# Optimization experiments

Measured on AMD Instinct MI355X. Metric: run time of the kernel, lower is better.

## Reference

```python
import jax, jax.numpy as jnp
import numpy as np
from jax import lax

SEQ, HIS, TGT = 4096, 32768, 2048
LOC_E, TIM_E, HID, UID_E, UID_N = 512, 64, 512, 64, 100000
IN = LOC_E + TIM_E  # 576


def setup_inputs() -> dict:
    key = jax.random.key(0)
    ks = jax.random.split(key, 16)
    s = lambda *sh: 1.0 / np.sqrt(sh[-1])
    return {
        "loc_emb": jax.random.normal(ks[0], (SEQ, 1, LOC_E), jnp.float32),
        "tim_emb": jax.random.normal(ks[1], (SEQ, 1, TIM_E), jnp.float32),
        "history_loc_emb": jax.random.normal(ks[2], (HIS, 1, LOC_E), jnp.float32),
        "history_tim_emb": jax.random.normal(ks[3], (HIS, 1, TIM_E), jnp.float32),
        "history_count": jax.random.randint(ks[4], (HIS,), 0, 10),
        "uid": jax.random.randint(ks[5], (TGT,), 0, UID_N),
        "target_len": TGT,
        "batch_size": 1,
        "fc_attn_w": jax.random.normal(ks[6], (HID, IN), jnp.float32) * s(HID, IN),
        "fc_attn_b": jnp.zeros((HID,), jnp.float32),
        "w_ih": jax.random.normal(ks[7], (3 * HID, IN), jnp.float32) * s(3 * HID, IN),
        "w_hh": jax.random.normal(ks[8], (3 * HID, HID), jnp.float32) * s(3 * HID, HID),
        "b_ih": jnp.zeros((3 * HID,), jnp.float32),
        "b_hh": jnp.zeros((3 * HID,), jnp.float32),
        "emb_uid": jax.random.normal(ks[9], (UID_N, UID_E), jnp.float32),
        "fc_final_w": jax.random.normal(ks[10], (LOC_E, 2 * HID + UID_E), jnp.float32) * s(LOC_E, 2 * HID + UID_E),
        "fc_final_b": jnp.zeros((LOC_E,), jnp.float32),
    }


def reference(loc_emb, tim_emb, history_loc_emb, history_tim_emb, history_count,
              uid, target_len, batch_size, fc_attn_w, fc_attn_b,
              w_ih, w_hh, b_ih, b_hh, emb_uid, fc_final_w, fc_final_b):
    hid = w_hh.shape[1]
    # current trajectory input: (S, IN); batch dim is 1 -> squeeze
    x = jnp.concatenate([loc_emb, tim_emb], axis=2)[:, 0, :]
    # long-term history projected to hidden: (L, HID)
    hist = jnp.concatenate([history_loc_emb, history_tim_emb], axis=2)[:, 0, :]
    history = jnp.tanh(hist @ fc_attn_w.T + fc_attn_b)

    # GRU (PyTorch gate layout: r, z, n). Precompute input projections once.
    gi = x @ w_ih.T + b_ih  # (S, 3*HID)

    def step(h, gi_t):
        gh = h @ w_hh.T + b_hh
        i_r, i_z, i_n = jnp.split(gi_t, 3)
        h_r, h_z, h_n = jnp.split(gh, 3)
        r = jax.nn.sigmoid(i_r + h_r)
        z = jax.nn.sigmoid(i_z + h_z)
        n = jnp.tanh(i_n + r * h_n)
        h_new = (1.0 - z) * n + z * h
        return h_new, h_new

    h0 = jnp.zeros((hid,), x.dtype)
    _, out_state = lax.scan(step, h0, gi)  # (S, HID)

    q = out_state[-target_len:]                 # (T, HID)
    # dot-product attention over history (batched matmul instead of scalar loop)
    attn_w = jax.nn.softmax(q @ history.T, axis=1)   # (T, L)
    context = attn_w @ history                       # (T, HID)

    out = jnp.concatenate([q, context], axis=1)      # (T, 2*HID)
    uid_e = emb_uid[uid]                             # (T, UID_E)
    out = jnp.concatenate([out, uid_e], axis=1)
    y = out @ fc_final_w.T + fc_final_b              # (T, LOC_E)
    return jax.nn.log_softmax(y, axis=1)
```

## Files before the change

kernel.cpp:

```cpp
#include <hip/hip_runtime.h>

using short8  = __attribute__((ext_vector_type(8))) short;
using float4v = __attribute__((ext_vector_type(4))) float;

__device__ __forceinline__ unsigned short f2b(float f){
  unsigned u = __float_as_uint(f);
  u += 0x7FFFu + ((u >> 16) & 1u);
  return (unsigned short)(u >> 16);
}
__device__ __forceinline__ float b2f(unsigned short h){
  return __uint_as_float(((unsigned)h) << 16);
}
__device__ __forceinline__ float sigm(float x){ return 1.f/(1.f + __expf(-x)); }
__device__ __forceinline__ float tanh_f(float x){
  float cx = fminf(fmaxf(x, -15.f), 15.f);
  float e = __expf(2.f*cx);
  return (e - 1.f)/(e + 1.f);
}

#define SENT64 0x7F8000007F800000ULL

__global__ void ring_init(unsigned long long* ring){
  size_t i = (size_t)blockIdx.x*256 + threadIdx.x;
  if (i < 512) ring[i] = 0ull;
  else ring[i] = SENT64;
}

__global__ void cat_hist(const float* __restrict__ a, const float* __restrict__ b,
                         unsigned short* __restrict__ d){
  int r = blockIdx.x;
  const float* ar = a + (size_t)r*512;
  const float* br = b + (size_t)r*64;
  unsigned short* dr = d + (size_t)r*576;
  for (int c = threadIdx.x; c < 576; c += 64){
    float v = (c < 512) ? ar[c] : br[c-512];
    dr[c] = f2b(v);
  }
}

__global__ void cat_x3(const float* __restrict__ a, const float* __restrict__ b,
                       unsigned short* __restrict__ d){
  int r = blockIdx.x;
  const float* ar = a + (size_t)r*512;
  const float* br = b + (size_t)r*64;
  unsigned short* dr = d + (size_t)r*1728;
  for (int c = threadIdx.x; c < 576; c += 64){
    float v = (c < 512) ? ar[c] : br[c-512];
    unsigned short hi = f2b(v);
    unsigned short lo = f2b(v - b2f(hi));
    dr[c] = hi; dr[576+c] = lo; dr[1152+c] = hi;
  }
}

__global__ void cat_w3(const float* __restrict__ w, unsigned short* __restrict__ d){
  int r = blockIdx.x;
  const float* wr_ = w + (size_t)r*576;
  unsigned short* dr = d + (size_t)r*1728;
  for (int c = threadIdx.x; c < 576; c += 64){
    float v = wr_[c];
    unsigned short hi = f2b(v);
    unsigned short lo = f2b(v - b2f(hi));
    dr[c] = hi; dr[576+c] = hi; dr[1152+c] = lo;
  }
}

__global__ void cast_bf16_k(const float* __restrict__ s, unsigned short* __restrict__ d, int n){
  int i = blockIdx.x*256 + threadIdx.x;
  if (i < n) d[i] = f2b(s[i]);
}

__global__ void transpose_k(const unsigned short* __restrict__ src,
                            unsigned short* __restrict__ dst, int R, int C){
  __shared__ unsigned short t[32][33];
  int x = threadIdx.x & 31, y = threadIdx.x >> 5;
  int r0 = blockIdx.y*32, c0 = blockIdx.x*32;
  for (int p=0;p<4;++p) t[y+p*8][x] = src[(size_t)(r0+y+p*8)*C + c0+x];
  __syncthreads();
  for (int p=0;p<4;++p) dst[(size_t)(c0+y+p*8)*R + r0+x] = t[x][y+p*8];
}

__global__ void uid_gather(const int* __restrict__ uid, const float* __restrict__ emb,
                           unsigned short* __restrict__ outcat){
  int r = blockIdx.x, e = threadIdx.x;
  outcat[(size_t)r*1088 + 1024 + e] = f2b(emb[(size_t)uid[r]*64 + e]);
}

template<int ACT>
__global__ __launch_bounds__(256) void gemm_bt(
  const unsigned short* __restrict__ A, const unsigned short* __restrict__ B,
  const float* __restrict__ bias, float* __restrict__ Cf, unsigned short* __restrict__ Cb,
  int M, int N, int K)
{
  __shared__ unsigned short As[64*40];
  __shared__ unsigned short Bs[64*40];
  const int tid  = threadIdx.x;
  const int lane = tid & 63, wave = tid >> 6;
  const int wr = (wave>>1)*32, wc = (wave&1)*32;
  const int qa = lane>>4, la = lane&15;
  const int arow = tid>>2, acol = (tid&3)*8;
  const int tiles = K >> 5;
  const size_t abase = (size_t)(blockIdx.x*64 + arow)*K + acol;
  const size_t bbase = (size_t)(blockIdx.y*64 + arow)*K + acol;
  float4v acc[2][2] = {};
  short8 av = *(const short8*)(A + abase);
  short8 bv = *(const short8*)(B + bbase);
  for (int kt=0; kt<tiles; ++kt){
    __syncthreads();
    *(short8*)(As + arow*40 + acol) = av;
    *(short8*)(Bs + arow*40 + acol) = bv;
    __syncthreads();
    if (kt+1 < tiles){
      av = *(const short8*)(A + abase + (size_t)(kt+1)*32);
      bv = *(const short8*)(B + bbase + (size_t)(kt+1)*32);
    }
    short8 af0 = *(const short8*)(As + (wr+la)*40 + qa*8);
    short8 af1 = *(const short8*)(As + (wr+16+la)*40 + qa*8);
    short8 bf0 = *(const short8*)(Bs + (wc+la)*40 + qa*8);
    short8 bf1 = *(const short8*)(Bs + (wc+16+la)*40 + qa*8);
    acc[0][0] = __builtin_amdgcn_mfma_f32_16x16x32_bf16(af0, bf0, acc[0][0],0,0,0);
    acc[0][1] = __builtin_amdgcn_mfma_f32_16x16x32_bf16(af0, bf1, acc[0][1],0,0,0);
    acc[1][0] = __builtin_amdgcn_mfma_f32_16x16x32_bf16(af1, bf0, acc[1][0],0,0,0);
    acc[1][1] = __builtin_amdgcn_mfma_f32_16x16x32_bf16(af1, bf1, acc[1][1],0,0,0);
  }
  for (int mi=0;mi<2;++mi) for (int ni=0;ni<2;++ni){
    int n = blockIdx.y*64 + wc + ni*16 + la;
    float bvv = bias ? bias[n] : 0.f;
    for (int r=0;r<4;++r){
      int m = blockIdx.x*64 + wr + mi*16 + qa*4 + r;
      float v = acc[mi][ni][r] + bvv;
      if (ACT) v = tanh_f(v);
      if (Cf) Cf[(size_t)m*N + n] = v;
      if (Cb) Cb[(size_t)m*N + n] = f2b(v);
    }
  }
}

__global__ __launch_bounds__(64,1) void gru_scan(
  const float* __restrict__ gi, const float* __restrict__ whh, const float* __restrict__ bhh,
  unsigned long long* ring, unsigned short* __restrict__ outcat)
{
  const int lane = threadIdx.x;
  const int b = blockIdx.x;
  const int ob = b*8;
  float wgt[24][8];
  #pragma unroll
  for (int s=0; s<24; ++s){
    const float* wr_ = whh + (size_t)((s>>3)*512 + ob + (s&7))*512 + lane*8;
    #pragma unroll
    for (int m=0; m<8; ++m) wgt[s][m] = wr_[m];
  }
  float bh = 0.f;
  if (lane < 24) bh = bhh[(lane>>3)*512 + ob + (lane&7)];
  float hprev = 0.f;

  const int bit0=lane&1, bit1=(lane>>1)&1, bit2=(lane>>2)&1,
            bit3=(lane>>3)&1, bit4=(lane>>4)&1;

  for (int t=0; t<4096; ++t){
    float gval = 0.f;
    if (lane < 24) gval = gi[(size_t)t*1536 + (lane>>3)*512 + ob + (lane&7)];
    const unsigned long long* rc = ring + (size_t)t*512 + lane*8;
    unsigned long long a0,a1,a2,a3;
    for(;;){
      a0 = __hip_atomic_load(rc+0, __ATOMIC_RELAXED, __HIP_MEMORY_SCOPE_AGENT);
      a1 = __hip_atomic_load(rc+1, __ATOMIC_RELAXED, __HIP_MEMORY_SCOPE_AGENT);
      a2 = __hip_atomic_load(rc+2, __ATOMIC_RELAXED, __HIP_MEMORY_SCOPE_AGENT);
      a3 = __hip_atomic_load(rc+3, __ATOMIC_RELAXED, __HIP_MEMORY_SCOPE_AGENT);
      bool bad = (a0==SENT64)|(a1==SENT64)|(a2==SENT64)|(a3==SENT64);
      if (!__any(bad)) break;
    }
    float hv[8];
    hv[0]=__uint_as_float((unsigned)a0); hv[1]=__uint_as_float((unsigned)(a0>>32));
    hv[2]=__uint_as_float((unsigned)a1); hv[3]=__uint_as_float((unsigned)(a1>>32));
    hv[4]=__uint_as_float((unsigned)a2); hv[5]=__uint_as_float((unsigned)(a2>>32));
    hv[6]=__uint_as_float((unsigned)a3); hv[7]=__uint_as_float((unsigned)(a3>>32));
    float v[32];
    #pragma unroll
    for (int s=0; s<24; ++s){
      float acc = 0.f;
      #pragma unroll
      for (int m=0; m<8; ++m) acc += wgt[s][m]*hv[m];
      v[s] = acc;
    }
    #pragma unroll
    for (int s=24; s<32; ++s) v[s] = 0.f;
    float s16[16];
    #pragma unroll
    for (int j=0; j<16; ++j){
      float keep = bit0 ? v[2*j+1] : v[2*j];
      float send = bit0 ? v[2*j]   : v[2*j+1];
      s16[j] = keep + __shfl_xor(send, 1, 64);
    }
    float s8[8];
    #pragma unroll
    for (int j=0; j<8; ++j){
      float keep = bit1 ? s16[2*j+1] : s16[2*j];
      float send = bit1 ? s16[2*j]   : s16[2*j+1];
      s8[j] = keep + __shfl_xor(send, 2, 64);
    }
    float s4[4];
    #pragma unroll
    for (int j=0; j<4; ++j){
      float keep = bit2 ? s8[2*j+1] : s8[2*j];
      float send = bit2 ? s8[2*j]   : s8[2*j+1];
      s4[j] = keep + __shfl_xor(send, 4, 64);
    }
    float s2[2];
    #pragma unroll
    for (int j=0; j<2; ++j){
      float keep = bit3 ? s4[2*j+1] : s4[2*j];
      float send = bit3 ? s4[2*j]   : s4[2*j+1];
      s2[j] = keep + __shfl_xor(send, 8, 64);
    }
    {
      float keep = bit4 ? s2[1] : s2[0];
      float send = bit4 ? s2[0] : s2[1];
      s2[0] = keep + __shfl_xor(send, 16, 64);
    }
    float vsum = s2[0] + __shfl_xor(s2[0], 32, 64);
    float wsum = vsum + bh;
    float wrz  = wsum + gval;
    float uz  = __shfl(wrz,  lane+8,  64);
    float hn  = __shfl(wsum, lane+16, 64);
    float in_ = __shfl(gval, lane+16, 64);
    float hval = 0.f;
    if (lane < 8){
      float r = sigm(wrz);
      float z = sigm(uz);
      float n = tanh_f(in_ + r*hn);
      hval = (1.f - z)*n + z*hprev;
      hprev = hval;
    }
    float nb = __shfl_xor(hval, 1, 64);
    if (lane < 8 && !(lane & 1)){
      unsigned long long pack = (unsigned long long)__float_as_uint(hval)
                              | ((unsigned long long)__float_as_uint(nb) << 32);
      __hip_atomic_store(ring + (size_t)(t+1)*512 + b*8 + (lane>>1), pack,
                         __ATOMIC_RELAXED, __HIP_MEMORY_SCOPE_AGENT);
      if (t >= 2048){
        unsigned opack = (unsigned)f2b(hval) | ((unsigned)f2b(nb) << 16);
        *(unsigned*)(outcat + (size_t)(t-2048)*1088 + ob + lane) = opack;
      }
    }
  }
}

__global__ __launch_bounds__(256) void attn_stats(
  const unsigned short* __restrict__ Q, const unsigned short* __restrict__ H,
  float* __restrict__ mpart, float* __restrict__ lpart)
{
  __shared__ unsigned short qs[64*520];
  const int tid = threadIdx.x;
  const int lane = tid&63, wave = tid>>6;
  const int qa = lane>>4, la = lane&15;
  const int qt = blockIdx.x, sp = blockIdx.y;
  for (int p=0;p<16;++p){
    int idx = p*256 + tid;
    int row = idx>>6, c8 = (idx&63)*8;
    *(short8*)(qs + row*520 + c8) = *(const short8*)(Q + (size_t)(qt*64+row)*1088 + c8);
  }
  __syncthreads();
  const int rowbase = wave*16;
  float mrun[4] = {-3e38f,-3e38f,-3e38f,-3e38f};
  float lrun[4] = {0.f,0.f,0.f,0.f};
  for (int c=0;c<32;++c){
    int hb = sp*2048 + c*64;
    float4v sacc[4] = {};
    for (int ks=0; ks<16; ++ks){
      short8 af = *(const short8*)(qs + (rowbase+la)*520 + ks*32 + qa*8);
      #pragma unroll
      for (int ni=0; ni<4; ++ni){
        short8 bf = *(const short8*)(H + (size_t)(hb + ni*16 + la)*512 + ks*32 + qa*8);
        sacc[ni] = __builtin_amdgcn_mfma_f32_16x16x32_bf16(af, bf, sacc[ni],0,0,0);
      }
    }
    #pragma unroll
    for (int r=0;r<4;++r){
      float cm = fmaxf(fmaxf(sacc[0][r],sacc[1][r]), fmaxf(sacc[2][r],sacc[3][r]));
      cm = fmaxf(cm, __shfl_xor(cm,1,64));
      cm = fmaxf(cm, __shfl_xor(cm,2,64));
      cm = fmaxf(cm, __shfl_xor(cm,4,64));
      cm = fmaxf(cm, __shfl_xor(cm,8,64));
      float mnew = fmaxf(mrun[r], cm);
      float ls = __expf(sacc[0][r]-mnew)+__expf(sacc[1][r]-mnew)
               + __expf(sacc[2][r]-mnew)+__expf(sacc[3][r]-mnew);
      ls += __shfl_xor(ls,1,64); ls += __shfl_xor(ls,2,64);
      ls += __shfl_xor(ls,4,64); ls += __shfl_xor(ls,8,64);
      lrun[r] = lrun[r]*__expf(mrun[r]-mnew) + ls;
      mrun[r] = mnew;
    }
  }
  if (la == 0){
    #pragma unroll
    for (int r=0;r<4;++r){
      int row = qt*64 + rowbase + qa*4 + r;
      mpart[sp*2048 + row] = mrun[r];
      lpart[sp*2048 + row] = lrun[r];
    }
  }
}

__global__ void stats_combine(const float* __restrict__ mpart, const float* __restrict__ lpart,
                              float* __restrict__ mrow, float* __restrict__ lrow){
  int r = blockIdx.x*64 + threadIdx.x;
  float m = -3e38f;
  for (int s=0;s<16;++s) m = fmaxf(m, mpart[s*2048 + r]);
  float l = 0.f;
  for (int s=0;s<16;++s) l += lpart[s*2048 + r]*__expf(mpart[s*2048 + r] - m);
  mrow[r] = m; lrow[r] = l;
}

__global__ __launch_bounds__(256) void attn_ctx(
  const unsigned short* __restrict__ Q, const unsigned short* __restrict__ H,
  const unsigned short* __restrict__ Ht, const float* __restrict__ mrow,
  float* __restrict__ ctxpart)
{
  __shared__ unsigned short qs[64*520];
  __shared__ unsigned short ps[4*16*80];
  const int tid = threadIdx.x;
  const int lane = tid&63, wave = tid>>6;
  const int qa = lane>>4, la = lane&15;
  const int qt = blockIdx.x, sp = blockIdx.y;
  for (int p=0;p<16;++p){
    int idx = p*256 + tid;
    int row = idx>>6, c8 = (idx&63)*8;
    *(short8*)(qs + row*520 + c8) = *(const short8*)(Q + (size_t)(qt*64+row)*1088 + c8);
  }
  __syncthreads();
  const int rowbase = wave*16;
  float mreg[4];
  #pragma unroll
  for (int r=0;r<4;++r) mreg[r] = mrow[qt*64 + rowbase + qa*4 + r];
  float4v cacc[32] = {};
  unsigned short* pw = ps + wave*16*80;
  for (int c=0;c<64;++c){
    int hb = sp*4096 + c*64;
    float4v sacc[4] = {};
    for (int ks=0; ks<16; ++ks){
      short8 af = *(const short8*)(qs + (rowbase+la)*520 + ks*32 + qa*8);
      #pragma unroll
      for (int ni=0; ni<4; ++ni){
        short8 bf = *(const short8*)(H + (size_t)(hb + ni*16 + la)*512 + ks*32 + qa*8);
        sacc[ni] = __builtin_amdgcn_mfma_f32_16x16x32_bf16(af, bf, sacc[ni],0,0,0);
      }
    }
    #pragma unroll
    for (int ni=0;ni<4;++ni)
      #pragma unroll
      for (int r=0;r<4;++r)
        pw[(qa*4+r)*80 + ni*16 + la] = f2b(__expf(sacc[ni][r]-mreg[r]));
    #pragma unroll
    for (int ks2=0; ks2<2; ++ks2){
      short8 paf = *(const short8*)(pw + la*80 + ks2*32 + qa*8);
      for (int f=0; f<32; ++f){
        short8 bf = *(const short8*)(Ht + (size_t)(f*16+la)*32768 + hb + ks2*32 + qa*8);
        cacc[f] = __builtin_amdgcn_mfma_f32_16x16x32_bf16(paf, bf, cacc[f],0,0,0);
      }
    }
  }
  for (int f=0; f<32; ++f)
    #pragma unroll
    for (int r=0;r<4;++r){
      int row = qt*64 + rowbase + qa*4 + r;
      ctxpart[((size_t)sp*2048 + row)*512 + f*16 + la] = cacc[f][r];
    }
}

__global__ void ctx_reduce(const float* __restrict__ ctxpart, const float* __restrict__ lrow,
                           unsigned short* __restrict__ outcat){
  int idx = blockIdx.x*256 + threadIdx.x;
  int r = idx >> 9, cc = idx & 511;
  float s = 0.f;
  for (int sp=0; sp<8; ++sp) s += ctxpart[((size_t)sp*2048 + r)*512 + cc];
  outcat[(size_t)r*1088 + 512 + cc] = f2b(s / lrow[r]);
}

__global__ void log_softmax_k(const float* __restrict__ y, float* __restrict__ out){
  int r = blockIdx.x, lane = threadIdx.x;
  const float* yr = y + (size_t)r*512;
  float v[8]; float m = -3e38f;
  #pragma unroll
  for (int i=0;i<8;++i){ v[i] = yr[lane + 64*i]; m = fmaxf(m, v[i]); }
  #pragma unroll
  for (int d=1; d<64; d<<=1) m = fmaxf(m, __shfl_xor(m,d,64));
  float s = 0.f;
  #pragma unroll
  for (int i=0;i<8;++i) s += __expf(v[i]-m);
  #pragma unroll
  for (int d=1; d<64; d<<=1) s += __shfl_xor(s,d,64);
  float ls = __logf(s) + m;
  float* orow = out + (size_t)r*512;
  #pragma unroll
  for (int i=0;i<8;++i) orow[lane + 64*i] = v[i] - ls;
}

extern "C" void kernel_launch(void* const* d_in, const int* in_sizes, int n_in,
                              void* d_out, int out_size, void* d_ws, size_t ws_size,
                              hipStream_t stream)
{
  const float* loc  = (const float*)d_in[0];
  const float* tim  = (const float*)d_in[1];
  const float* hloc = (const float*)d_in[2];
  const float* htim = (const float*)d_in[3];
  const int*   uid  = (const int*)d_in[5];
  const float* fc_attn_w  = (const float*)d_in[8];
  const float* fc_attn_b  = (const float*)d_in[9];
  const float* w_ih = (const float*)d_in[10];
  const float* w_hh = (const float*)d_in[11];
  const float* b_ih = (const float*)d_in[12];
  const float* b_hh = (const float*)d_in[13];
  const float* emb_uid    = (const float*)d_in[14];
  const float* fc_final_w = (const float*)d_in[15];
  const float* fc_final_b = (const float*)d_in[16];
  float* out = (float*)d_out;

  char* ws = (char*)d_ws;
  size_t off = 0;
  auto alloc = [&](size_t b){ size_t o = off; off = (off + b + 255) & ~(size_t)255; return o; };
  size_t o_xcat3 = alloc(4096ULL*1728*2);
  size_t o_hist  = alloc(32768ULL*576*2);
  size_t o_wAb   = alloc(512ULL*576*2);
  size_t o_wIb3  = alloc(1536ULL*1728*2);
  size_t o_wFb   = alloc(512ULL*1088*2);
  size_t o_H     = alloc(32768ULL*512*2);
  size_t o_Ht    = alloc(32768ULL*512*2);
  size_t o_gi    = alloc(4096ULL*1536*4);
  size_t o_outc  = alloc(2048ULL*1088*2);
  size_t o_ring  = alloc(4097ULL*512*8);
  size_t o_mp    = alloc(16*2048*4);
  size_t o_lp    = alloc(16*2048*4);
  size_t o_mr    = alloc(2048*4);
  size_t o_lr    = alloc(2048*4);
  (void)ws_size; (void)in_sizes; (void)n_in; (void)out_size;

  unsigned short* xcat3   = (unsigned short*)(ws + o_xcat3);
  unsigned short* histcat = (unsigned short*)(ws + o_hist);
  unsigned short* wAb     = (unsigned short*)(ws + o_wAb);
  unsigned short* wIb3    = (unsigned short*)(ws + o_wIb3);
  unsigned short* wFb     = (unsigned short*)(ws + o_wFb);
  unsigned short* Hb      = (unsigned short*)(ws + o_H);
  unsigned short* Htb     = (unsigned short*)(ws + o_Ht);
  float*          gi      = (float*)(ws + o_gi);
  unsigned short* outc    = (unsigned short*)(ws + o_outc);
  unsigned long long* ring = (unsigned long long*)(ws + o_ring);
  float*          mp      = (float*)(ws + o_mp);
  float*          lp      = (float*)(ws + o_lp);
  float*          mr      = (float*)(ws + o_mr);
  float*          lr      = (float*)(ws + o_lr);
  float*          y       = (float*)(ws + o_xcat3);
  float*          ctxpart = (float*)(ws + o_hist);

  ring_init<<<8194, 256, 0, stream>>>(ring);
  cat_x3<<<4096, 64, 0, stream>>>(loc, tim, xcat3);
  cat_hist<<<32768, 64, 0, stream>>>(hloc, htim, histcat);
  cast_bf16_k<<<(294912+255)/256, 256, 0, stream>>>(fc_attn_w, wAb, 294912);
  cat_w3<<<1536, 64, 0, stream>>>(w_ih, wIb3);
  cast_bf16_k<<<(557056+255)/256, 256, 0, stream>>>(fc_final_w, wFb, 557056);

  gemm_bt<1><<<dim3(512,8), 256, 0, stream>>>(histcat, wAb, fc_attn_b, nullptr, Hb, 32768, 512, 576);
  transpose_k<<<dim3(16,1024), 256, 0, stream>>>(Hb, Htb, 32768, 512);
  gemm_bt<0><<<dim3(64,24), 256, 0, stream>>>(xcat3, wIb3, b_ih, gi, nullptr, 4096, 1536, 1728);
  gru_scan<<<64, 64, 0, stream>>>(gi, w_hh, b_hh, ring, outc);
  attn_stats<<<dim3(32,16), 256, 0, stream>>>(outc, Hb, mp, lp);
  stats_combine<<<32, 64, 0, stream>>>(mp, lp, mr, lr);
  attn_ctx<<<dim3(32,8), 256, 0, stream>>>(outc, Hb, Htb, mr, ctxpart);
  ctx_reduce<<<4096, 256, 0, stream>>>(ctxpart, lr, outc);
  uid_gather<<<2048, 64, 0, stream>>>(uid, emb_uid, outc);
  gemm_bt<0><<<dim3(32,8), 256, 0, stream>>>(outc, wFb, fc_final_b, y, nullptr, 2048, 512, 1088);
  log_softmax_k<<<2048, 64, 0, stream>>>(y, out);
}
```

Measured before the change: 10.47 ms.

## Repack GRU input projections per block and prefetch ring/gi lines in scan

Adds a repack kernel that lays out the GRU input projections so each scan block reads its 24 gate values contiguously. Inside the serial scan, every 8 steps it issues dummy loads of future ring slots and future gi rows to warm the caches. The spin-wait is also changed so each lane stops reloading once its own values are ready, which cuts redundant atomic traffic. The repack kernel adds a pass over gi, and the prefetch loads add work on the critical recurrent path.

Result: slower. 11.12 ms (+6.1%).

```diff
diff --git a/kernel.cpp b/kernel.cpp
--- a/kernel.cpp
+++ b/kernel.cpp
@@ -67,6 +67,15 @@
 __global__ void cast_bf16_k(const float* __restrict__ s, unsigned short* __restrict__ d, int n){
   int i = blockIdx.x*256 + threadIdx.x;
   if (i < n) d[i] = f2b(s[i]);
+}
+
+__global__ void gi_repack(const float* __restrict__ gi, float* __restrict__ gp){
+  int t = blockIdx.x;
+  for (int k = threadIdx.x; k < 1536; k += 256){
+    int b = k / 24, rem = k - b*24;
+    int g = rem >> 3, jj = rem & 7;
+    gp[(size_t)t*1536 + k] = gi[(size_t)t*1536 + g*512 + b*8 + jj];
+  }
 }
 
 __global__ void transpose_k(const unsigned short* __restrict__ src,
@@ -136,7 +145,7 @@
 }
 
 __global__ __launch_bounds__(64,1) void gru_scan(
-  const float* __restrict__ gi, const float* __restrict__ whh, const float* __restrict__ bhh,
+  const float* __restrict__ gp, const float* __restrict__ whh, const float* __restrict__ bhh,
   unsigned long long* ring, unsigned short* __restrict__ outcat)
 {
   const int lane = threadIdx.x;
@@ -158,16 +167,37 @@
 
   for (int t=0; t<4096; ++t){
     float gval = 0.f;
-    if (lane < 24) gval = gi[(size_t)t*1536 + (lane>>3)*512 + ob + (lane&7)];
+    if (lane < 24) gval = gp[(size_t)t*1536 + b*24 + lane];
     const unsigned long long* rc = ring + (size_t)t*512 + lane*8;
-    unsigned long long a0,a1,a2,a3;
+    unsigned long long a0=0,a1=0,a2=0,a3=0;
+    bool done = false;
     for(;;){
-      a0 = __hip_atomic_load(rc+0, __ATOMIC_RELAXED, __HIP_MEMORY_SCOPE_AGENT);
-      a1 = __hip_atomic_load(rc+1, __ATOMIC_RELAXED, __HIP_MEMORY_SCOPE_AGENT);
-      a2 = __hip_atomic_load(rc+2, __ATOMIC_RELAXED, __HIP_MEMORY_SCOPE_AGENT);
-      a3 = __hip_atomic_load(rc+3, __ATOMIC_RELAXED, __HIP_MEMORY_SCOPE_AGENT);
-      bool bad = (a0==SENT64)|(a1==SENT64)|(a2==SENT64)|(a3==SENT64);
-      if (!__any(bad)) break;
+      if (!done){
+        a0 = __hip_atomic_load(rc+0, __ATOMIC_RELAXED, __HIP_MEMORY_SCOPE_AGENT);
+        a1 = __hip_atomic_load(rc+1, __ATOMIC_RELAXED, __HIP_MEMORY_SCOPE_AGENT);
+        a2 = __hip_atomic_load(rc+2, __ATOMIC_RELAXED, __HIP_MEMORY_SCOPE_AGENT);
+        a3 = __hip_atomic_load(rc+3, __ATOMIC_RELAXED, __HIP_MEMORY_SCOPE_AGENT);
+        done = !((a0==SENT64)|(a1==SENT64)|(a2==SENT64)|(a3==SENT64));
+      }
+      if (__all(done)) break;
+    }
+    if ((t & 7) == 0){
+      unsigned long long wacc = 0;
+      #pragma unroll
+      for (int k=0; k<8; ++k){
+        int s = t+9+k; s = s > 4096 ? 4096 : s;
+        wacc ^= __hip_atomic_load(ring + (size_t)s*512 + lane*8,
+                                  __ATOMIC_RELAXED, __HIP_MEMORY_SCOPE_AGENT);
+      }
+      float gacc = 0.f;
+      if (lane < 24){
+        #pragma unroll
+        for (int k=0; k<8; ++k){
+          int s = t+8+k; s = s > 4095 ? 4095 : s;
+          gacc += gp[(size_t)s*1536 + b*24 + lane];
+        }
+      }
+      asm volatile("" : "+v"(wacc), "+v"(gacc));
     }
     float hv[8];
     hv[0]=__uint_as_float((unsigned)a0); hv[1]=__uint_as_float((unsigned)(a0>>32));
@@ -448,6 +478,7 @@
   float*          mr      = (float*)(ws + o_mr);
   float*          lr      = (float*)(ws + o_lr);
   float*          y       = (float*)(ws + o_xcat3);
+  float*          gp      = (float*)(ws + o_hist);
   float*          ctxpart = (float*)(ws + o_hist);
 
   ring_init<<<8194, 256, 0, stream>>>(ring);
@@ -460,7 +491,8 @@
   gemm_bt<1><<<dim3(512,8), 256, 0, stream>>>(histcat, wAb, fc_attn_b, nullptr, Hb, 32768, 512, 576);
   transpose_k<<<dim3(16,1024), 256, 0, stream>>>(Hb, Htb, 32768, 512);
   gemm_bt<0><<<dim3(64,24), 256, 0, stream>>>(xcat3, wIb3, b_ih, gi, nullptr, 4096, 1536, 1728);
-  gru_scan<<<64, 64, 0, stream>>>(gi, w_hh, b_hh, ring, outc);
+  gi_repack<<<4096, 256, 0, stream>>>(gi, gp);
+  gru_scan<<<64, 64, 0, stream>>>(gp, w_hh, b_hh, ring, outc);
   attn_stats<<<dim3(32,16), 256, 0, stream>>>(outc, Hb, mp, lp);
   stats_combine<<<32, 64, 0, stream>>>(mp, lp, mr, lr);
   attn_ctx<<<dim3(32,8), 256, 0, stream>>>(outc, Hb, Htb, mr, ctxpart);
```
